# Optimization experiments

Hardware: AMD Instinct MI355X
Metric: run time of the kernel (lower is better)

The kernel has to match this reference:

```python
import jax, jax.numpy as jnp
import numpy as np

N = 100000      # nodes
E = 800000      # edges
F_IN = 128      # input feature dim
HID = 8         # per-head hidden
HEADS = 8
HD = HID * HEADS  # 64
G = 128         # graphs in batch
C = 10          # classes
SLOPE = 0.2     # leaky relu negative slope


def setup_inputs() -> dict:
    key = jax.random.key(0)
    ks = iter(jax.random.split(key, 48))
    def rn(shape, scale=0.1):
        return jax.random.normal(next(ks), shape, jnp.float32) * scale
    inp = {
        'x': jax.random.normal(next(ks), (N, F_IN), jnp.float32),
        'edge_index': jax.random.randint(next(ks), (2, E), 0, N),
        'batch': jnp.sort(jax.random.randint(next(ks), (N,), 0, G)),
        # GAT layer 1
        'W1': rn((F_IN, HEADS * HID)), 'as1': rn((HEADS, HID)), 'ad1': rn((HEADS, HID)), 'b1': jnp.zeros((HEADS * HID,), jnp.float32),
        # GAT layer 2
        'W2': rn((HD, HEADS * HID)), 'as2': rn((HEADS, HID)), 'ad2': rn((HEADS, HID)), 'b2': jnp.zeros((HEADS * HID,), jnp.float32),
        # node attention MLP (HD -> HD//2 -> 2)
        'na_w1': rn((HD, HD // 2)), 'na_b1': jnp.zeros((HD // 2,), jnp.float32), 'na_w2': rn((HD // 2, 2)), 'na_b2': jnp.zeros((2,), jnp.float32),
        # edge attention MLP (2*HD -> HD -> 2)
        'ea_w1': rn((2 * HD, HD)), 'ea_b1': jnp.zeros((HD,), jnp.float32), 'ea_w2': rn((HD, 2)), 'ea_b2': jnp.zeros((2,), jnp.float32),
        # GCN causal / trivial
        'gc_w': rn((HD, HD)), 'gc_b': jnp.zeros((HD,), jnp.float32),
        'gt_w': rn((HD, HD)), 'gt_b': jnp.zeros((HD,), jnp.float32),
        # readouts
        'rc_w': rn((HD, HD)), 'rc_b': jnp.zeros((HD,), jnp.float32),
        'rt_w': rn((HD, HD)), 'rt_b': jnp.zeros((HD,), jnp.float32),
        # classifiers (HD -> HD//2 -> C), combined (2HD -> HD -> C)
        'cc_w1': rn((HD, HD // 2)), 'cc_b1': jnp.zeros((HD // 2,), jnp.float32), 'cc_w2': rn((HD // 2, C)), 'cc_b2': jnp.zeros((C,), jnp.float32),
        'ct_w1': rn((HD, HD // 2)), 'ct_b1': jnp.zeros((HD // 2,), jnp.float32), 'ct_w2': rn((HD // 2, C)), 'ct_b2': jnp.zeros((C,), jnp.float32),
        'cm_w1': rn((2 * HD, HD)), 'cm_b1': jnp.zeros((HD,), jnp.float32), 'cm_w2': rn((HD, C)), 'cm_b2': jnp.zeros((C,), jnp.float32),
    }
    return inp


def _mlp2(h, w1, b1, w2, b2):
    return jax.nn.relu(h @ w1 + b1) @ w2 + b2


def reference(x, edge_index, batch,
              W1, as1, ad1, b1, W2, as2, ad2, b2,
              na_w1, na_b1, na_w2, na_b2,
              ea_w1, ea_b1, ea_w2, ea_b2,
              gc_w, gc_b, gt_w, gt_b,
              rc_w, rc_b, rt_w, rt_b,
              cc_w1, cc_b1, cc_w2, cc_b2,
              ct_w1, ct_b1, ct_w2, ct_b2,
              cm_w1, cm_b1, cm_w2, cm_b2):
    src, dst = edge_index[0], edge_index[1]
    loop = jnp.arange(N)
    s2 = jnp.concatenate([src, loop])  # edges + self-loops (PyG GATConv/GCNConv add self-loops)
    d2 = jnp.concatenate([dst, loop])

    def gat(h_in, W, a_s, a_d, b):
        h = (h_in @ W).reshape(N, HEADS, HID)
        es = jnp.einsum('nhd,hd->nh', h, a_s)
        ed = jnp.einsum('nhd,hd->nh', h, a_d)
        logit = jax.nn.leaky_relu(es[s2] + ed[d2], SLOPE)      # [E+N, H]
        m = jax.ops.segment_max(logit, d2, num_segments=N)
        ex = jnp.exp(logit - m[d2])
        den = jax.ops.segment_sum(ex, d2, num_segments=N)
        alpha = ex / (den[d2] + 1e-16)
        out = jax.ops.segment_sum(h[s2] * alpha[..., None], d2, num_segments=N)
        return out.reshape(N, HEADS * HID) + b

    # GNN encoder (dropout disabled: eval mode)
    H1 = jax.nn.elu(gat(x, W1, as1, ad1, b1))
    H = gat(H1, W2, as2, ad2, b2)                              # [N, HD]

    # node attention
    na = jax.nn.softmax(_mlp2(H, na_w1, na_b1, na_w2, na_b2), axis=1)
    alpha_c, alpha_t = na[:, 0], na[:, 1]
    # edge attention (original edges, no self-loops)
    ef = jnp.concatenate([H[src], H[dst]], axis=1)             # [E, 2*HD]
    ea = jax.nn.softmax(_mlp2(ef, ea_w1, ea_b1, ea_w2, ea_b2), axis=1)
    beta_c, beta_t = ea[:, 0], ea[:, 1]

    Hc = H * alpha_c[:, None]
    Ht = H * alpha_t[:, None]

    def gcn(h_in, w, b, ew):
        # PyG gcn_norm: self-loops with weight 1, symmetric deg^-1/2 normalization
        w_full = jnp.concatenate([ew, jnp.ones((N,), h_in.dtype)])
        deg = jax.ops.segment_sum(w_full, d2, num_segments=N)
        dis = jnp.where(deg > 0, jax.lax.rsqrt(jnp.maximum(deg, 1e-20)), 0.0)
        norm = dis[s2] * w_full * dis[d2]
        h = h_in @ w
        return jax.ops.segment_sum(h[s2] * norm[:, None], d2, num_segments=N) + b

    Gc = gcn(Hc, gc_w, gc_b, beta_c)
    Gt = gcn(Ht, gt_w, gt_b, beta_t)

    # readout: linear then global_add_pool
    hGc = jax.ops.segment_sum(Gc @ rc_w + rc_b, batch, num_segments=G)  # [G, HD]
    hGt = jax.ops.segment_sum(Gt @ rt_w + rt_b, batch, num_segments=G)

    zc = _mlp2(hGc, cc_w1, cc_b1, cc_w2, cc_b2)
    zt = _mlp2(hGt, ct_w1, ct_b1, ct_w2, ct_b2)
    # RandomIntervention: within-graph node shuffle followed by add-pool == plain add-pool
    h_comb = jnp.concatenate([hGc + hGt], axis=1) if False else (hGc + hGt)
    zp = _mlp2(jnp.concatenate([h_comb, jnp.zeros_like(h_comb)], axis=1), cm_w1, cm_b1, cm_w2, cm_b2) if False else _mlp2_comb(h_comb, cm_w1, cm_b1, cm_w2, cm_b2)
    return (zc, zt, zp, hGc, hGt)


def _mlp2_comb(h_comb, cm_w1, cm_b1, cm_w2, cm_b2):
    # original: classifier_combined takes hidden_dim*2 input; forward feeds h_G_c + shuffled_h_G_t
    # which is [G, HD]; to match Linear(2*HD, ...) we use the first HD rows of cm_w1 twice?
    # NO -- the original code as written passes a [G, HD] tensor to a Linear(2*HD, HD) layer,
    # which would error in torch. Faithful runnable interpretation: combined feature is
    # concat([h_G_c, shuffled_h_G_t]) of width 2*HD (the standard CAL formulation).
    return jax.nn.relu(h_comb @ cm_w1 + cm_b1) @ cm_w2 + cm_b2


# clean final definition overriding the commented exploration above
def reference(x, edge_index, batch,
              W1, as1, ad1, b1, W2, as2, ad2, b2,
              na_w1, na_b1, na_w2, na_b2,
              ea_w1, ea_b1, ea_w2, ea_b2,
              gc_w, gc_b, gt_w, gt_b,
              rc_w, rc_b, rt_w, rt_b,
              cc_w1, cc_b1, cc_w2, cc_b2,
              ct_w1, ct_b1, ct_w2, ct_b2,
              cm_w1, cm_b1, cm_w2, cm_b2):
    src, dst = edge_index[0], edge_index[1]
    loop = jnp.arange(N)
    s2 = jnp.concatenate([src, loop])
    d2 = jnp.concatenate([dst, loop])

    def gat(h_in, W, a_s, a_d, b):
        h = (h_in @ W).reshape(N, HEADS, HID)
        es = jnp.einsum('nhd,hd->nh', h, a_s)
        ed = jnp.einsum('nhd,hd->nh', h, a_d)
        logit = jax.nn.leaky_relu(es[s2] + ed[d2], SLOPE)
        m = jax.ops.segment_max(logit, d2, num_segments=N)
        ex = jnp.exp(logit - m[d2])
        den = jax.ops.segment_sum(ex, d2, num_segments=N)
        alpha = ex / (den[d2] + 1e-16)
        out = jax.ops.segment_sum(h[s2] * alpha[..., None], d2, num_segments=N)
        return out.reshape(N, HEADS * HID) + b

    H1 = jax.nn.elu(gat(x, W1, as1, ad1, b1))
    H = gat(H1, W2, as2, ad2, b2)

    na = jax.nn.softmax(_mlp2(H, na_w1, na_b1, na_w2, na_b2), axis=1)
    alpha_c, alpha_t = na[:, 0], na[:, 1]
    ef = jnp.concatenate([H[src], H[dst]], axis=1)
    ea = jax.nn.softmax(_mlp2(ef, ea_w1, ea_b1, ea_w2, ea_b2), axis=1)
    beta_c, beta_t = ea[:, 0], ea[:, 1]

    Hc = H * alpha_c[:, None]
    Ht = H * alpha_t[:, None]

    def gcn(h_in, w, b, ew):
        w_full = jnp.concatenate([ew, jnp.ones((N,), h_in.dtype)])
        deg = jax.ops.segment_sum(w_full, d2, num_segments=N)
        dis = jnp.where(deg > 0, jax.lax.rsqrt(jnp.maximum(deg, 1e-20)), 0.0)
        norm = dis[s2] * w_full * dis[d2]
        h = h_in @ w
        return jax.ops.segment_sum(h[s2] * norm[:, None], d2, num_segments=N) + b

    Gc = gcn(Hc, gc_w, gc_b, beta_c)
    Gt = gcn(Ht, gt_w, gt_b, beta_t)

    hGc = jax.ops.segment_sum(Gc @ rc_w + rc_b, batch, num_segments=G)
    hGt = jax.ops.segment_sum(Gt @ rt_w + rt_b, batch, num_segments=G)

    zc = _mlp2(hGc, cc_w1, cc_b1, cc_w2, cc_b2)
    zt = _mlp2(hGt, ct_w1, ct_b1, ct_w2, ct_b2)
    # RandomIntervention with sorted batch: within-graph permutation + add-pool == add-pool
    h_comb = jnp.concatenate([hGc, hGt], axis=1)  # [G, 2*HD] for Linear(2*HD, ...)
    zp = _mlp2(h_comb, cm_w1, cm_b1, cm_w2, cm_b2)
    return (zc, zt, zp, hGc, hGt)


if __name__ == '__main__':
    out = reference(**setup_inputs())
    print([o.shape for o in out])
```

## Files before the change

kernel.cpp:

```cpp
#include <hip/hip_runtime.h>
#include <hip/hip_bf16.h>

#define N_NODES 100000
#define E_EDGES 800000
#define E2 (E_EDGES + N_NODES)
#define FIN 128
#define HD 64
#define NH 8
#define NG 128
#define NC 10
#define SLOPE 0.2f
#define SELF_FLAG 0x40000000
#define SRC_MASK  0x3FFFFFFF
#define NSCAN_BLK 391
#define NBLK64 1563
#define GB 16
#define ECAP 256
#define NPW 4
#define EA_BLKS 6250

#define U1_STRIPES 261
#define U1_GRID (2 + U1_STRIPES * 7)
#define U1_HISTB (U1_STRIPES * 4)
#define T1 (U1_STRIPES * 3)
#define U2_STRIPES 391
#define U2_GRID (U2_STRIPES * 11)

typedef unsigned short bfu;

__device__ __forceinline__ float lrelu(float x) { return x > 0.f ? x : SLOPE * x; }

__device__ __forceinline__ bfu f2bf(float f) {
    unsigned int u = __float_as_uint(f);
    u += 0x7FFFu + ((u >> 16) & 1u);
    return (bfu)(u >> 16);
}
__device__ __forceinline__ float bf2f(bfu s) {
    return __uint_as_float(((unsigned int)s) << 16);
}
__device__ __forceinline__ float bflo(unsigned int u) { return __uint_as_float(u << 16); }
__device__ __forceinline__ float bfhi(unsigned int u) { return __uint_as_float(u & 0xFFFF0000u); }

template<typename TIN, int KIN, int MODE>
__device__ __forceinline__
void gemm_tile_body(float* smem, int tile,
                    const TIN* __restrict__ in, const float* __restrict__ W,
                    bfu* __restrict__ outB,
                    const float* __restrict__ a_s, const float* __restrict__ a_d,
                    float* __restrict__ es, float* __restrict__ ed)
{
    constexpr int KH = (KIN > 64) ? 64 : KIN;
    constexpr int RS = KIN + 4;
    float* Ws   = smem;
    float* rows = smem + KH * 64;
    int t = threadIdx.x;
    int base = tile * 64;

    if constexpr (sizeof(TIN) == 4) {
        constexpr int RQ = KIN / 4;
        for (int i = t; i < 64 * RQ; i += 256) {
            int r = i / RQ, c = (i % RQ) * 4;
            int n = base + r;
            float4 v = make_float4(0.f, 0.f, 0.f, 0.f);
            if (n < N_NODES) v = *(const float4*)((const float*)in + (size_t)n * KIN + c);
            *(float4*)(rows + r * RS + c) = v;
        }
    } else {
        constexpr int RQ = KIN / 8;
        for (int i = t; i < 64 * RQ; i += 256) {
            int r = i / RQ, c = (i % RQ) * 8;
            int n = base + r;
            uint4 v = make_uint4(0, 0, 0, 0);
            if (n < N_NODES) v = *(const uint4*)((const bfu*)in + (size_t)n * KIN + c);
            float* dp = rows + r * RS + c;
            *(float4*)dp       = make_float4(bflo(v.x), bfhi(v.x), bflo(v.y), bfhi(v.y));
            *(float4*)(dp + 4) = make_float4(bflo(v.z), bfhi(v.z), bflo(v.w), bfhi(v.w));
        }
    }

    int tr = t >> 4, tc = t & 15;
    float acc[4][4] = {};
    const float4* R4 = (const float4*)rows;

    for (int h = 0; h < KIN / KH; ++h) {
        __syncthreads();
        {
            const float4* Wv = (const float4*)(W + (size_t)h * KH * 64);
            float4* Wsv4 = (float4*)Ws;
            for (int i = t; i < KH * 16; i += 256) Wsv4[i] = Wv[i];
        }
        __syncthreads();
        const float4* Wsv = (const float4*)Ws;
#pragma unroll 2
        for (int k = 0; k < KH; k += 4) {
            float4 w0 = Wsv[(k + 0) * 16 + tc];
            float4 w1 = Wsv[(k + 1) * 16 + tc];
            float4 w2 = Wsv[(k + 2) * 16 + tc];
            float4 w3 = Wsv[(k + 3) * 16 + tc];
            int kq = (h * KH + k) >> 2;
#pragma unroll
            for (int i = 0; i < 4; ++i) {
                float4 r = R4[(tr * 4 + i) * (RS / 4) + kq];
                acc[i][0] = fmaf(r.x, w0.x, fmaf(r.y, w1.x, fmaf(r.z, w2.x, fmaf(r.w, w3.x, acc[i][0]))));
                acc[i][1] = fmaf(r.x, w0.y, fmaf(r.y, w1.y, fmaf(r.z, w2.y, fmaf(r.w, w3.y, acc[i][1]))));
                acc[i][2] = fmaf(r.x, w0.z, fmaf(r.y, w1.z, fmaf(r.z, w2.z, fmaf(r.w, w3.z, acc[i][2]))));
                acc[i][3] = fmaf(r.x, w0.w, fmaf(r.y, w1.w, fmaf(r.z, w2.w, fmaf(r.w, w3.w, acc[i][3]))));
            }
        }
    }

    int j0 = tc * 4;
#pragma unroll
    for (int i = 0; i < 4; ++i) {
        int n = base + tr * 4 + i;
        if (n < N_NODES) {
            ushort4 ov;
            ov.x = f2bf(acc[i][0]); ov.y = f2bf(acc[i][1]);
            ov.z = f2bf(acc[i][2]); ov.w = f2bf(acc[i][3]);
            *(ushort4*)(outB + (size_t)n * 64 + j0) = ov;
        }
    }
    if (MODE == 1) {
        float s0[4], s1[4];
#pragma unroll
        for (int i = 0; i < 4; ++i) {
            float pes = 0.f, ped = 0.f;
#pragma unroll
            for (int q = 0; q < 4; ++q) {
                pes = fmaf(acc[i][q], a_s[j0 + q], pes);
                ped = fmaf(acc[i][q], a_d[j0 + q], ped);
            }
            pes += __shfl_xor(pes, 1, 64);
            ped += __shfl_xor(ped, 1, 64);
            s0[i] = pes; s1[i] = ped;
        }
        if ((tc & 1) == 0) {
            int h = tc >> 1;
#pragma unroll
            for (int i = 0; i < 4; ++i) {
                int n = base + tr * 4 + i;
                if (n < N_NODES) {
                    es[n * NH + h] = s0[i];
                    ed[n * NH + h] = s1[i];
                }
            }
        }
    }
}

__device__ __forceinline__
void weight_prep_body(float* smem,
                      const float* __restrict__ gw, const float* __restrict__ gb,
                      const float* __restrict__ rw, const float* __restrict__ rb,
                      float* __restrict__ Wp, float* __restrict__ bp)
{
    float* A = smem;
    float* B = smem + 4096;
    int t = threadIdx.x;
    {
        const float4* ga = (const float4*)gw;
        const float4* rA = (const float4*)rw;
        float4* dA = (float4*)A; float4* dB = (float4*)B;
        for (int i = t; i < 1024; i += 256) { dA[i] = ga[i]; dB[i] = rA[i]; }
    }
    __syncthreads();
    for (int e = t * 16; e < t * 16 + 16; ++e) {
        int k = e >> 6, j = e & 63;
        float acc = 0.f;
#pragma unroll 8
        for (int m = 0; m < 64; ++m) acc = fmaf(A[k * 64 + m], B[m * 64 + j], acc);
        Wp[e] = acc;
    }
    if (t < 64) {
        float acc = rb[t];
#pragma unroll 8
        for (int m = 0; m < 64; ++m) acc = fmaf(gb[m], B[m * 64 + t], acc);
        bp[t] = acc;
    }
}

__global__ __launch_bounds__(256)
void u1_fused(const float* __restrict__ x, const float* __restrict__ W1,
              bfu* __restrict__ B0, const float* __restrict__ as1,
              const float* __restrict__ ad1, float* __restrict__ es,
              float* __restrict__ ed,
              const int* __restrict__ ei, int* __restrict__ cnt,
              int* __restrict__ rank,
              const float* __restrict__ gc_w, const float* __restrict__ gc_b,
              const float* __restrict__ rc_w, const float* __restrict__ rc_b,
              const float* __restrict__ gt_w, const float* __restrict__ gt_b,
              const float* __restrict__ rt_w, const float* __restrict__ rt_b,
              float* __restrict__ Wcp, float* __restrict__ bcp,
              float* __restrict__ Wtp, float* __restrict__ btp)
{
    __shared__ __align__(16) float smem[12544];
    int b = blockIdx.x;
    if (b < 2) {
        if (b == 0) weight_prep_body(smem, gc_w, gc_b, rc_w, rc_b, Wcp, bcp);
        else        weight_prep_body(smem, gt_w, gt_b, rt_w, rt_b, Wtp, btp);
        return;
    }
    int u = b - 2;
    int stripe = u / 7, r = u % 7;
    if (r < 3) {
        gemm_tile_body<float, FIN, 1>(smem, stripe * 3 + r, x, W1, B0, as1, ad1, es, ed);
    } else {
        int idx = stripe * 4 + (r - 3);
        int t = threadIdx.x;
        const int STR = U1_HISTB * 256;
        for (int e = idx * 256 + t; e < E_EDGES; e += 2 * STR) {
            int e1 = e + STR;
            int d0 = ei[E_EDGES + e];
            int r0 = atomicAdd(&cnt[d0], 1);
            int r1 = 0;
            bool has1 = e1 < E_EDGES;
            if (has1) r1 = atomicAdd(&cnt[ei[E_EDGES + e1]], 1);
            rank[e] = r0;
            if (has1) rank[e1] = r1;
        }
    }
}

__global__ __launch_bounds__(256)
void u2_fused(const float* __restrict__ x, const float* __restrict__ W1,
              bfu* __restrict__ B0, const float* __restrict__ as1,
              const float* __restrict__ ad1, float* __restrict__ es,
              float* __restrict__ ed,
              const int* __restrict__ ei, const int* __restrict__ rank,
              const int* __restrict__ offs,
              int* __restrict__ csr)
{
    __shared__ __align__(16) float smem[12544];
    int b = blockIdx.x;
    int stripe = b / 11, r = b % 11;
    int t = threadIdx.x;
    if (r < 8) {
        int e = (stripe * 8 + r) * 256 + t;
        if (e < E_EDGES) {
            int s = ei[e], d = ei[E_EDGES + e];
            csr[offs[d] + rank[e]] = s;
        }
    } else if (r < 10) {
        int tile = T1 + stripe * 2 + (r - 8);
        if (tile < NBLK64)
            gemm_tile_body<float, FIN, 1>(smem, tile, x, W1, B0, as1, ad1, es, ed);
    } else {
        int n = stripe * 256 + t;
        if (n < N_NODES) {
            csr[offs[n + 1] - 1] = n | SELF_FLAG;
        }
    }
}

__global__ __launch_bounds__(256)
void u3_fused(const bfu* __restrict__ in,
              const float* __restrict__ na_w1, const float* __restrict__ na_b1,
              const float* __restrict__ na_w2, const float* __restrict__ na_b2,
              float2* __restrict__ al2,
              const float* __restrict__ ea_w1,
              bfu* __restrict__ out0, bfu* __restrict__ out1)
{
    __shared__ __align__(16) float smem[12544];
    float* Ws   = smem;
    float* rows = smem + 8192;
    int t = threadIdx.x;
    int base = blockIdx.x * 64;
    const float* W0 = ea_w1;
    const float* W1 = ea_w1 + 64 * 64;
    {
        const float4* W0v = (const float4*)W0;
        const float4* W1v = (const float4*)W1;
        float4* Wsv = (float4*)Ws;
        for (int i = t; i < 1024; i += 256) { Wsv[i] = W0v[i]; Wsv[1024 + i] = W1v[i]; }
    }
    for (int i = t; i < 64 * 8; i += 256) {
        int r = i >> 3, c = (i & 7) * 8;
        int n = base + r;
        uint4 v = make_uint4(0, 0, 0, 0);
        if (n < N_NODES) v = *(const uint4*)(in + (size_t)n * 64 + c);
        float* dp = rows + r * 68 + c;
        *(float4*)dp       = make_float4(bflo(v.x), bfhi(v.x), bflo(v.y), bfhi(v.y));
        *(float4*)(dp + 4) = make_float4(bflo(v.z), bfhi(v.z), bflo(v.w), bfhi(v.w));
    }
    __syncthreads();
    {
        int tr = t >> 4, tc = t & 15;
        float a0[4][4] = {}, a1[4][4] = {};
        const float4* Wsv = (const float4*)Ws;
        const float4* R4 = (const float4*)rows;
#pragma unroll 2
        for (int k = 0; k < 64; k += 4) {
            float4 p0 = Wsv[(k + 0) * 16 + tc];
            float4 p1 = Wsv[(k + 1) * 16 + tc];
            float4 p2 = Wsv[(k + 2) * 16 + tc];
            float4 p3 = Wsv[(k + 3) * 16 + tc];
            float4 q0 = Wsv[1024 + (k + 0) * 16 + tc];
            float4 q1 = Wsv[1024 + (k + 1) * 16 + tc];
            float4 q2 = Wsv[1024 + (k + 2) * 16 + tc];
            float4 q3 = Wsv[1024 + (k + 3) * 16 + tc];
            int kq = k >> 2;
#pragma unroll
            for (int i = 0; i < 4; ++i) {
                float4 r = R4[(tr * 4 + i) * 17 + kq];
                a0[i][0] = fmaf(r.x, p0.x, fmaf(r.y, p1.x, fmaf(r.z, p2.x, fmaf(r.w, p3.x, a0[i][0]))));
                a0[i][1] = fmaf(r.x, p0.y, fmaf(r.y, p1.y, fmaf(r.z, p2.y, fmaf(r.w, p3.y, a0[i][1]))));
                a0[i][2] = fmaf(r.x, p0.z, fmaf(r.y, p1.z, fmaf(r.z, p2.z, fmaf(r.w, p3.z, a0[i][2]))));
                a0[i][3] = fmaf(r.x, p0.w, fmaf(r.y, p1.w, fmaf(r.z, p2.w, fmaf(r.w, p3.w, a0[i][3]))));
                a1[i][0] = fmaf(r.x, q0.x, fmaf(r.y, q1.x, fmaf(r.z, q2.x, fmaf(r.w, q3.x, a1[i][0]))));
                a1[i][1] = fmaf(r.x, q0.y, fmaf(r.y, q1.y, fmaf(r.z, q2.y, fmaf(r.w, q3.y, a1[i][1]))));
                a1[i][2] = fmaf(r.x, q0.z, fmaf(r.y, q1.z, fmaf(r.z, q2.z, fmaf(r.w, q3.z, a1[i][2]))));
                a1[i][3] = fmaf(r.x, q0.w, fmaf(r.y, q1.w, fmaf(r.z, q2.w, fmaf(r.w, q3.w, a1[i][3]))));
            }
        }
        int j0 = tc * 4;
#pragma unroll
        for (int i = 0; i < 4; ++i) {
            int n = base + tr * 4 + i;
            if (n >= N_NODES) continue;
            ushort4 o0, o1;
            o0.x = f2bf(a0[i][0]); o0.y = f2bf(a0[i][1]);
            o0.z = f2bf(a0[i][2]); o0.w = f2bf(a0[i][3]);
            o1.x = f2bf(a1[i][0]); o1.y = f2bf(a1[i][1]);
            o1.z = f2bf(a1[i][2]); o1.w = f2bf(a1[i][3]);
            *(ushort4*)(out0 + (size_t)n * 64 + j0) = o0;
            *(ushort4*)(out1 + (size_t)n * 64 + j0) = o1;
        }
    }
    __syncthreads();
    {
        const float4* w1v = (const float4*)na_w1;
        float4* dst = (float4*)Ws;
        for (int i = t; i < 512; i += 256) dst[i] = w1v[i];
        if (t < 64) Ws[2048 + t] = na_w2[t];
    }
    __syncthreads();
    {
        int tr = t >> 3;
        int tc = t & 7;
        float4 bv = *(const float4*)(na_b1 + tc * 4);
        float4 acc0 = bv, acc1 = bv;
        const float4* w1sv = (const float4*)Ws;
#pragma unroll 8
        for (int k = 0; k < 64; ++k) {
            float4 w = w1sv[k * 8 + tc];
            float r0 = rows[tr * 68 + k];
            float r1 = rows[(tr + 32) * 68 + k];
            acc0.x = fmaf(r0, w.x, acc0.x); acc0.y = fmaf(r0, w.y, acc0.y);
            acc0.z = fmaf(r0, w.z, acc0.z); acc0.w = fmaf(r0, w.w, acc0.w);
            acc1.x = fmaf(r1, w.x, acc1.x); acc1.y = fmaf(r1, w.y, acc1.y);
            acc1.z = fmaf(r1, w.z, acc1.z); acc1.w = fmaf(r1, w.w, acc1.w);
        }
        float z00 = 0.f, z01 = 0.f, z10 = 0.f, z11 = 0.f;
        float h0, w20, w21;
        int j0 = tc * 4;
#pragma unroll
        for (int q = 0; q < 4; ++q) {
            float a0q = q == 0 ? acc0.x : q == 1 ? acc0.y : q == 2 ? acc0.z : acc0.w;
            float a1q = q == 0 ? acc1.x : q == 1 ? acc1.y : q == 2 ? acc1.z : acc1.w;
            w20 = Ws[2048 + (j0 + q) * 2]; w21 = Ws[2048 + (j0 + q) * 2 + 1];
            h0 = fmaxf(a0q, 0.f);
            z00 = fmaf(h0, w20, z00); z01 = fmaf(h0, w21, z01);
            h0 = fmaxf(a1q, 0.f);
            z10 = fmaf(h0, w20, z10); z11 = fmaf(h0, w21, z11);
        }
#pragma unroll
        for (int o = 1; o < 8; o <<= 1) {
            z00 += __shfl_xor(z00, o, 64); z01 += __shfl_xor(z01, o, 64);
            z10 += __shfl_xor(z10, o, 64); z11 += __shfl_xor(z11, o, 64);
        }
        if (tc == 0) {
            int n0 = base + tr, n1 = base + tr + 32;
            if (n0 < N_NODES) {
                float zz0 = z00 + na_b2[0], zz1 = z01 + na_b2[1];
                float mx = fmaxf(zz0, zz1);
                float e0 = __expf(zz0 - mx), e1 = __expf(zz1 - mx);
                float ss = e0 + e1;
                al2[n0] = make_float2(e0 / ss, e1 / ss);
            }
            if (n1 < N_NODES) {
                float zz0 = z10 + na_b2[0], zz1 = z11 + na_b2[1];
                float mx = fmaxf(zz0, zz1);
                float e0 = __expf(zz0 - mx), e1 = __expf(zz1 - mx);
                float ss = e0 + e1;
                al2[n1] = make_float2(e0 / ss, e1 / ss);
            }
        }
    }
}

__global__ __launch_bounds__(256)
void gemm_tile_k64(const bfu* __restrict__ in, const float* __restrict__ W,
                   bfu* __restrict__ outB,
                   const float* __restrict__ a_s, const float* __restrict__ a_d,
                   float* __restrict__ es, float* __restrict__ ed)
{
    __shared__ __align__(16) float smem[64 * 64 + 64 * 68];
    gemm_tile_body<bfu, 64, 1>(smem, blockIdx.x, in, W, outB, a_s, a_d, es, ed);
}

__global__ void csr_scan1(const int* __restrict__ cnt, int* __restrict__ offs,
                          int* __restrict__ bsum, const int* __restrict__ batch,
                          int* __restrict__ glo)
{
    __shared__ int tmp[256];
    int t = threadIdx.x;
    int i = blockIdx.x * 256 + t;
    int v = (i < N_NODES) ? cnt[i] + 1 : 0;
    tmp[t] = v; __syncthreads();
#pragma unroll
    for (int o = 1; o < 256; o <<= 1) {
        int a = (t >= o) ? tmp[t - o] : 0;
        __syncthreads();
        tmp[t] += a;
        __syncthreads();
    }
    if (i < N_NODES) offs[i] = tmp[t] - v;
    if (t == 255) bsum[blockIdx.x] = tmp[255];
    if (blockIdx.x == 0 && t <= NG) {
        int l = 0, r = N_NODES;
        while (l < r) { int m = (l + r) >> 1; if (batch[m] < t) l = m + 1; else r = m; }
        glo[t] = l;
    }
}

__global__ void csr_scan23(int* __restrict__ offs, const int* __restrict__ bsum)
{
    __shared__ int tmp[256];
    int b = blockIdx.x;
    int t = threadIdx.x;
    int s = 0;
    for (int j = t; j < b; j += 256) s += bsum[j];
    tmp[t] = s; __syncthreads();
#pragma unroll
    for (int o = 128; o > 0; o >>= 1) {
        if (t < o) tmp[t] += tmp[t + o];
        __syncthreads();
    }
    int prefix = tmp[0];
    int i = b * 256 + t;
    if (i < N_NODES) offs[i] += prefix;
    if (i == 0) offs[N_NODES] = E2;
}

template<int ELU>
__global__ void gat_aggregate4(const int* __restrict__ offs, const int* __restrict__ csr,
                               const float* __restrict__ es, const float* __restrict__ ed,
                               const bfu* __restrict__ hsrcB, const float* __restrict__ bias,
                               bfu* __restrict__ outB)
{
    int n = blockIdx.x * 4 + (threadIdx.x >> 6);
    int lane = threadIdx.x & 63;
    if (n >= N_NODES) return;
    int g  = lane >> 4;
    int fl = lane & 15;
    int h  = fl >> 1;
    int beg = offs[n], end = offs[n + 1];
    float edv = ed[n * NH + h];
    float den = 0.f;
    float4 acc = make_float4(0.f, 0.f, 0.f, 0.f);
    int p = beg + g;
    for (; p + 4 < end; p += 8) {
        int s0 = csr[p] & SRC_MASK;
        int s1 = csr[p + 4] & SRC_MASK;
        float l0 = lrelu(es[s0 * NH + h] + edv);
        float l1 = lrelu(es[s1 * NH + h] + edv);
        float ex0 = __expf(l0);
        float ex1 = __expf(l1);
        den += ex0 + ex1;
        ushort4 ra = *(const ushort4*)(hsrcB + (size_t)s0 * HD + fl * 4);
        ushort4 rb = *(const ushort4*)(hsrcB + (size_t)s1 * HD + fl * 4);
        acc.x = fmaf(bf2f(ra.x), ex0, fmaf(bf2f(rb.x), ex1, acc.x));
        acc.y = fmaf(bf2f(ra.y), ex0, fmaf(bf2f(rb.y), ex1, acc.y));
        acc.z = fmaf(bf2f(ra.z), ex0, fmaf(bf2f(rb.z), ex1, acc.z));
        acc.w = fmaf(bf2f(ra.w), ex0, fmaf(bf2f(rb.w), ex1, acc.w));
    }
    if (p < end) {
        int s = csr[p] & SRC_MASK;
        float l = lrelu(es[s * NH + h] + edv);
        float ex = __expf(l);
        den += ex;
        ushort4 rb = *(const ushort4*)(hsrcB + (size_t)s * HD + fl * 4);
        acc.x = fmaf(bf2f(rb.x), ex, acc.x);
        acc.y = fmaf(bf2f(rb.y), ex, acc.y);
        acc.z = fmaf(bf2f(rb.z), ex, acc.z);
        acc.w = fmaf(bf2f(rb.w), ex, acc.w);
    }
#pragma unroll
    for (int o = 16; o <= 32; o <<= 1) {
        den   += __shfl_xor(den,   o, 64);
        acc.x += __shfl_xor(acc.x, o, 64);
        acc.y += __shfl_xor(acc.y, o, 64);
        acc.z += __shfl_xor(acc.z, o, 64);
        acc.w += __shfl_xor(acc.w, o, 64);
    }
    if (g == 0) {
        float inv = 1.f / (den + 1e-16f);
        float4 bv = *(const float4*)(bias + fl * 4);
        float v0 = acc.x * inv + bv.x;
        float v1 = acc.y * inv + bv.y;
        float v2 = acc.z * inv + bv.z;
        float v3 = acc.w * inv + bv.w;
        if (ELU) {
            v0 = v0 > 0.f ? v0 : (__expf(v0) - 1.f);
            v1 = v1 > 0.f ? v1 : (__expf(v1) - 1.f);
            v2 = v2 > 0.f ? v2 : (__expf(v2) - 1.f);
            v3 = v3 > 0.f ? v3 : (__expf(v3) - 1.f);
        }
        ushort4 ov;
        ov.x = f2bf(v0); ov.y = f2bf(v1); ov.z = f2bf(v2); ov.w = f2bf(v3);
        *(ushort4*)(outB + (size_t)n * HD + fl * 4) = ov;
    }
}

__global__ __launch_bounds__(256)
void edge_att_node(const int* __restrict__ offs, const int* __restrict__ csr,
                   const bfu* __restrict__ P1b, const bfu* __restrict__ P2b,
                   const float* __restrict__ b1, const float* __restrict__ w2,
                   const float* __restrict__ b2,
                   const float2* __restrict__ al2,
                   float2* __restrict__ beta2,
                   float2* __restrict__ prod2)
{
    __shared__ float2 bbuf[4][ECAP];
    int w = threadIdx.x >> 6;
    int lane = threadIdx.x & 63;
    int nbase = (blockIdx.x * 4 + w) * NPW;
    if (nbase >= N_NODES) return;
    int slot = lane >> 3, q = lane & 7;
    const float4* pb = (const float4*)(b1 + q * 8);
    const float4* pw = (const float4*)(w2 + q * 16);
    float4 c0 = pb[0], c1 = pb[1];
    float4 w0 = pw[0], w1v = pw[1], w2v = pw[2], w3v = pw[3];
    float wd0 = w0.x - w0.y,   wd1 = w0.z - w0.w;
    float wd2 = w1v.x - w1v.y, wd3 = w1v.z - w1v.w;
    float wd4 = w2v.x - w2v.y, wd5 = w2v.z - w2v.w;
    float wd6 = w3v.x - w3v.y, wd7 = w3v.z - w3v.w;
    float zbd = b2[0] - b2[1];
    for (int j = 0; j < NPW; ++j) {
        int n = nbase + j;
        if (n >= N_NODES) return;
        uint4 U2 = *(const uint4*)(P2b + (size_t)n * 64 + q * 8);
        float d0 = bflo(U2.x) + c0.x, d1 = bfhi(U2.x) + c0.y;
        float d2 = bflo(U2.y) + c0.z, d3 = bfhi(U2.y) + c0.w;
        float d4 = bflo(U2.z) + c1.x, d5 = bfhi(U2.z) + c1.y;
        float d6 = bflo(U2.w) + c1.z, d7 = bfhi(U2.w) + c1.w;
        int beg = offs[n], endr = offs[n + 1] - 1;
        int m = endr - beg;
        float dc = 0.f, dt = 0.f;
        for (int p = beg + slot; p < endr; p += 8) {
            int s = csr[p];
            uint4 U1 = *(const uint4*)(P1b + (size_t)s * 64 + q * 8);
            float h0 = fmaxf(bflo(U1.x) + d0, 0.f);
            float h1 = fmaxf(bfhi(U1.x) + d1, 0.f);
            float h2 = fmaxf(bflo(U1.y) + d2, 0.f);
            float h3 = fmaxf(bfhi(U1.y) + d3, 0.f);
            float h4 = fmaxf(bflo(U1.z) + d4, 0.f);
            float h5 = fmaxf(bfhi(U1.z) + d5, 0.f);
            float h6 = fmaxf(bflo(U1.w) + d6, 0.f);
            float h7 = fmaxf(bfhi(U1.w) + d7, 0.f);
            float z = fmaf(h0, wd0, fmaf(h1, wd1, fmaf(h2, wd2, fmaf(h3, wd3,
                      fmaf(h4, wd4, fmaf(h5, wd5, fmaf(h6, wd6, h7 * wd7)))))));
            z += __shfl_xor(z, 1, 64);
            z += __shfl_xor(z, 2, 64);
            z += __shfl_xor(z, 4, 64);
            if (q == 0) {
                z += zbd;
                float e = __expf(-fabsf(z));
                float inv = 1.f / (1.f + e);
                float bx = z >= 0.f ? inv : e * inv;
                float by = z >= 0.f ? e * inv : inv;
                int idx = p - beg;
                if (idx < ECAP) bbuf[w][idx] = make_float2(bx, by);
                else            beta2[p]    = make_float2(bx, by);
                dc += bx; dt += by;
            }
        }
        dc += __shfl_xor(dc, 8, 64);  dt += __shfl_xor(dt, 8, 64);
        dc += __shfl_xor(dc, 16, 64); dt += __shfl_xor(dt, 16, 64);
        dc += __shfl_xor(dc, 32, 64); dt += __shfl_xor(dt, 32, 64);
        dc = __shfl(dc, 0, 64); dt = __shfl(dt, 0, 64);
        dc += 1.f; dt += 1.f;
        float ic = rsqrtf(fmaxf(dc, 1e-20f));
        float it = rsqrtf(fmaxf(dt, 1e-20f));
        if (lane == 0) {
            float2 al = al2[n];
            prod2[n] = make_float2(ic * al.x, it * al.y);
        }
        if (m > ECAP)
            asm volatile("s_waitcnt vmcnt(0)" ::: "memory");
        for (int idx = lane; idx <= m; idx += 64) {
            float2 v = (idx == m) ? make_float2(1.f, 1.f)
                     : (idx < ECAP) ? bbuf[w][idx] : beta2[beg + idx];
            beta2[beg + idx] = make_float2(v.x * ic, v.y * it);
        }
    }
}

__global__ __launch_bounds__(256)
void gcn_readout_fused(const int* __restrict__ offs, const int* __restrict__ csr,
                       const int* __restrict__ glo,
                       const bfu* __restrict__ HB,
                       const float2* __restrict__ beta2,
                       const float2* __restrict__ prod2,
                       float* __restrict__ Pc, float* __restrict__ Pt)
{
    int g = blockIdx.x / GB, b = blockIdx.x % GB;
    int t = threadIdx.x;
    int pbeg = offs[glo[g]], pend = offs[glo[g + 1]];
    int total = pend - pbeg;
    int chunk = (total + GB - 1) / GB;
    int start = pbeg + b * chunk;
    int end = start + chunk;
    if (end > pend) end = pend;
    if (start > pend) start = pend;
    int slot = t >> 4, fl = t & 15;
    float4 a1 = make_float4(0.f, 0.f, 0.f, 0.f);
    float4 a2 = make_float4(0.f, 0.f, 0.f, 0.f);
    int p = start + slot;
    for (; p + 48 < end; p += 64) {
#pragma unroll
        for (int j = 0; j < 4; ++j) {
            int pp = p + j * 16;
            int s = csr[pp] & SRC_MASK;
            float2 bb = beta2[pp];
            float2 pr = prod2[s];
            float wc = pr.x * bb.x;
            float wt = pr.y * bb.y;
            ushort4 r0 = *(const ushort4*)(HB + (size_t)s * HD + fl * 4);
            float f0 = bf2f(r0.x), f1 = bf2f(r0.y), f2 = bf2f(r0.z), f3 = bf2f(r0.w);
            a1.x = fmaf(f0, wc, a1.x); a1.y = fmaf(f1, wc, a1.y);
            a1.z = fmaf(f2, wc, a1.z); a1.w = fmaf(f3, wc, a1.w);
            a2.x = fmaf(f0, wt, a2.x); a2.y = fmaf(f1, wt, a2.y);
            a2.z = fmaf(f2, wt, a2.z); a2.w = fmaf(f3, wt, a2.w);
        }
    }
    for (; p < end; p += 16) {
        int s = csr[p] & SRC_MASK;
        float2 bb = beta2[p];
        float2 pr = prod2[s];
        float wc = pr.x * bb.x;
        float wt = pr.y * bb.y;
        ushort4 r0 = *(const ushort4*)(HB + (size_t)s * HD + fl * 4);
        float f0 = bf2f(r0.x), f1 = bf2f(r0.y), f2 = bf2f(r0.z), f3 = bf2f(r0.w);
        a1.x = fmaf(f0, wc, a1.x); a1.y = fmaf(f1, wc, a1.y);
        a1.z = fmaf(f2, wc, a1.z); a1.w = fmaf(f3, wc, a1.w);
        a2.x = fmaf(f0, wt, a2.x); a2.y = fmaf(f1, wt, a2.y);
        a2.z = fmaf(f2, wt, a2.z); a2.w = fmaf(f3, wt, a2.w);
    }
    __shared__ float redc[16 * 64], redt[16 * 64];
    *(float4*)(redc + slot * 64 + fl * 4) = a1;
    *(float4*)(redt + slot * 64 + fl * 4) = a2;
    __syncthreads();
    if (t < 64) {
        float sc = 0.f, st = 0.f;
#pragma unroll
        for (int s = 0; s < 16; ++s) { sc += redc[s * 64 + t]; st += redt[s * 64 + t]; }
        Pc[(size_t)blockIdx.x * 64 + t] = sc;
        Pt[(size_t)blockIdx.x * 64 + t] = st;
    }
}

__global__ __launch_bounds__(64)
void head_final(const float* __restrict__ Pc, const float* __restrict__ Pt,
                const int* __restrict__ glo,
                const float* __restrict__ Wcp, const float* __restrict__ bcp,
                const float* __restrict__ Wtp, const float* __restrict__ btp,
                const float* __restrict__ cc_w1, const float* __restrict__ cc_b1,
                const float* __restrict__ cc_w2, const float* __restrict__ cc_b2,
                const float* __restrict__ ct_w1, const float* __restrict__ ct_b1,
                const float* __restrict__ ct_w2, const float* __restrict__ ct_b2,
                const float* __restrict__ cm_w1, const float* __restrict__ cm_b1,
                const float* __restrict__ cm_w2, const float* __restrict__ cm_b2,
                float* __restrict__ out)
{
    int g = blockIdx.x;
    int t = threadIdx.x;
    __shared__ float scl[64], stl[64], hgc[64], hgt[64], hid[64];
    float sc = 0.f, st = 0.f;
#pragma unroll
    for (int b = 0; b < GB; ++b) {
        sc += Pc[(size_t)(g * GB + b) * 64 + t];
        st += Pt[(size_t)(g * GB + b) * 64 + t];
    }
    scl[t] = sc; stl[t] = st;
    float c = (float)(glo[g + 1] - glo[g]);
    __syncthreads();
    {
        float a = c * bcp[t], bb = c * btp[t];
#pragma unroll 8
        for (int k = 0; k < 64; ++k) {
            a  = fmaf(scl[k], Wcp[k * 64 + t], a);
            bb = fmaf(stl[k], Wtp[k * 64 + t], bb);
        }
        hgc[t] = a; hgt[t] = bb;
        out[3840 + g * 64 + t]  = a;
        out[12032 + g * 64 + t] = bb;
    }
    __syncthreads();
    if (t < 32) {
        float a = cc_b1[t];
#pragma unroll 8
        for (int k = 0; k < 64; ++k) a = fmaf(hgc[k], cc_w1[k * 32 + t], a);
        hid[t] = fmaxf(a, 0.f);
    }
    __syncthreads();
    if (t < NC) {
        float a = cc_b2[t];
#pragma unroll
        for (int k = 0; k < 32; ++k) a = fmaf(hid[k], cc_w2[k * NC + t], a);
        out[g * NC + t] = a;
    }
    __syncthreads();
    if (t < 32) {
        float a = ct_b1[t];
#pragma unroll 8
        for (int k = 0; k < 64; ++k) a = fmaf(hgt[k], ct_w1[k * 32 + t], a);
        hid[t] = fmaxf(a, 0.f);
    }
    __syncthreads();
    if (t < NC) {
        float a = ct_b2[t];
#pragma unroll
        for (int k = 0; k < 32; ++k) a = fmaf(hid[k], ct_w2[k * NC + t], a);
        out[1280 + g * NC + t] = a;
    }
    __syncthreads();
    {
        float a = cm_b1[t];
#pragma unroll 8
        for (int k = 0; k < 64; ++k) {
            a = fmaf(hgc[k], cm_w1[k * 64 + t], a);
            a = fmaf(hgt[k], cm_w1[(64 + k) * 64 + t], a);
        }
        hid[t] = fmaxf(a, 0.f);
    }
    __syncthreads();
    if (t < NC) {
        float a = cm_b2[t];
#pragma unroll 8
        for (int k = 0; k < 64; ++k) a = fmaf(hid[k], cm_w2[k * NC + t], a);
        out[2560 + g * NC + t] = a;
    }
}

extern "C" void kernel_launch(void* const* d_in, const int* in_sizes, int n_in,
                              void* d_out, int out_size, void* d_ws, size_t ws_size,
                              hipStream_t stream)
{
    const float* x     = (const float*)d_in[0];
    const int*   ei    = (const int*)d_in[1];
    const int*   batch = (const int*)d_in[2];
    const float* W1    = (const float*)d_in[3];
    const float* as1   = (const float*)d_in[4];
    const float* ad1   = (const float*)d_in[5];
    const float* b1    = (const float*)d_in[6];
    const float* W2    = (const float*)d_in[7];
    const float* as2   = (const float*)d_in[8];
    const float* ad2   = (const float*)d_in[9];
    const float* b2    = (const float*)d_in[10];
    const float* na_w1 = (const float*)d_in[11];
    const float* na_b1 = (const float*)d_in[12];
    const float* na_w2 = (const float*)d_in[13];
    const float* na_b2 = (const float*)d_in[14];
    const float* ea_w1 = (const float*)d_in[15];
    const float* ea_b1 = (const float*)d_in[16];
    const float* ea_w2 = (const float*)d_in[17];
    const float* ea_b2 = (const float*)d_in[18];
    const float* gc_w  = (const float*)d_in[19];
    const float* gc_b  = (const float*)d_in[20];
    const float* gt_w  = (const float*)d_in[21];
    const float* gt_b  = (const float*)d_in[22];
    const float* rc_w  = (const float*)d_in[23];
    const float* rc_b  = (const float*)d_in[24];
    const float* rt_w  = (const float*)d_in[25];
    const float* rt_b  = (const float*)d_in[26];
    const float* cc_w1 = (const float*)d_in[27];
    const float* cc_b1 = (const float*)d_in[28];
    const float* cc_w2 = (const float*)d_in[29];
    const float* cc_b2 = (const float*)d_in[30];
    const float* ct_w1 = (const float*)d_in[31];
    const float* ct_b1 = (const float*)d_in[32];
    const float* ct_w2 = (const float*)d_in[33];
    const float* ct_b2 = (const float*)d_in[34];
    const float* cm_w1 = (const float*)d_in[35];
    const float* cm_b1 = (const float*)d_in[36];
    const float* cm_w2 = (const float*)d_in[37];
    const float* cm_b2 = (const float*)d_in[38];
    float* out = (float*)d_out;

    float* ws = (float*)d_ws;
    size_t o = 0;
    const size_t nf = (size_t)N_NODES * HD;
    float* es    = ws + o; o += (size_t)N_NODES * NH;
    float* ed    = ws + o; o += (size_t)N_NODES * NH;
    float2* al2  = (float2*)(ws + o); o += (size_t)N_NODES * 2;
    float2* beta2= (float2*)(ws + o); o += (size_t)E2 * 2;
    float2* prod2= (float2*)(ws + o); o += (size_t)N_NODES * 2;
    bfu* B0      = (bfu*)(ws + o); o += nf / 2;
    bfu* B1      = (bfu*)(ws + o); o += nf / 2;
    bfu* B2      = (bfu*)(ws + o); o += nf / 2;
    bfu* BH1     = (bfu*)(ws + o); o += nf / 2;
    int* csr     = (int*)(ws + o); o += E2;
    int* offs    = (int*)(ws + o); o += N_NODES + 1;
    float* Pc    = ws + o; o += (size_t)NG * GB * 64;
    float* Pt    = ws + o; o += (size_t)NG * GB * 64;
    float* Wcp   = ws + o; o += 4096;
    float* Wtp   = ws + o; o += 4096;
    float* bcp   = ws + o; o += 64;
    float* btp   = ws + o; o += 64;
    int* glo     = (int*)(ws + o); o += NG + 2;
    int* cnt  = (int*)beta2;
    int* bsum = (int*)prod2;
    int* rank = (int*)B1;

    const int NW_BLKS = N_NODES / 4;

    hipMemsetAsync(cnt, 0, (size_t)N_NODES * 4, stream);
    u1_fused<<<U1_GRID, 256, 0, stream>>>(x, W1, B0, as1, ad1, es, ed,
                                          ei, cnt, rank,
                                          gc_w, gc_b, rc_w, rc_b,
                                          gt_w, gt_b, rt_w, rt_b,
                                          Wcp, bcp, Wtp, btp);
    csr_scan1<<<NSCAN_BLK, 256, 0, stream>>>(cnt, offs, bsum, batch, glo);
    csr_scan23<<<NSCAN_BLK, 256, 0, stream>>>(offs, bsum);

    u2_fused<<<U2_GRID, 256, 0, stream>>>(x, W1, B0, as1, ad1, es, ed,
                                          ei, rank, offs, csr);

    gat_aggregate4<1><<<NW_BLKS, 256, 0, stream>>>(offs, csr, es, ed, B0, b1, BH1);

    gemm_tile_k64<<<NBLK64, 256, 0, stream>>>(BH1, W2, B0, as2, ad2, es, ed);
    gat_aggregate4<0><<<NW_BLKS, 256, 0, stream>>>(offs, csr, es, ed, B0, b2, B2);

    u3_fused<<<NBLK64, 256, 0, stream>>>(B2, na_w1, na_b1, na_w2, na_b2, al2,
                                         ea_w1, B0, B1);

    edge_att_node<<<EA_BLKS, 256, 0, stream>>>(offs, csr, B0, B1,
                                               ea_b1, ea_w2, ea_b2, al2,
                                               beta2, prod2);

    gcn_readout_fused<<<NG * GB, 256, 0, stream>>>(offs, csr, glo, B2,
                                                   beta2, prod2, Pc, Pt);

    head_final<<<NG, 64, 0, stream>>>(Pc, Pt, glo,
                                      Wcp, bcp, Wtp, btp,
                                      cc_w1, cc_b1, cc_w2, cc_b2,
                                      ct_w1, ct_b1, ct_w2, ct_b2,
                                      cm_w1, cm_b1, cm_w2, cm_b2, out);
    (void)in_sizes; (void)n_in; (void)out_size; (void)ws_size;
}
```

Baseline: 465.5 us.

## Assign one 16-lane group per node in GAT aggregation instead of a whole wave

The GAT aggregation kernel used to give each node a full 64-lane wave, splitting that node's edges across four 16-lane groups and combining them with cross-lane shuffles. Now each 16-lane group owns its own node and walks all of its edges, two per iteration, so a block covers 16 nodes and the grid shrinks by four. This drops the shuffle reduction and the idle lanes during the write-out, and gives more independent nodes per wave. In exchange each group walks a longer serial edge chain, and groups in the same wave diverge when node degrees differ.

```diff
diff --git a/kernel.cpp b/kernel.cpp
--- a/kernel.cpp
+++ b/kernel.cpp
@@ -18,6 +18,7 @@
 #define ECAP 256
 #define NPW 4
 #define EA_BLKS 6250
+#define AG_BLKS 6250
 
 #define U1_STRIPES 261
 #define U1_GRID (2 + U1_STRIPES * 7)
@@ -448,24 +449,24 @@
                                const bfu* __restrict__ hsrcB, const float* __restrict__ bias,
                                bfu* __restrict__ outB)
 {
-    int n = blockIdx.x * 4 + (threadIdx.x >> 6);
+    int w = threadIdx.x >> 6;
     int lane = threadIdx.x & 63;
-    if (n >= N_NODES) return;
-    int g  = lane >> 4;
+    int slot = lane >> 4;
     int fl = lane & 15;
     int h  = fl >> 1;
+    int n = (blockIdx.x * 4 + w) * 4 + slot;
+    if (n >= N_NODES) return;
+    float4 bv = *(const float4*)(bias + fl * 4);
     int beg = offs[n], end = offs[n + 1];
     float edv = ed[n * NH + h];
     float den = 0.f;
     float4 acc = make_float4(0.f, 0.f, 0.f, 0.f);
-    int p = beg + g;
-    for (; p + 4 < end; p += 8) {
+    int p = beg;
+    for (; p + 1 < end; p += 2) {
         int s0 = csr[p] & SRC_MASK;
-        int s1 = csr[p + 4] & SRC_MASK;
-        float l0 = lrelu(es[s0 * NH + h] + edv);
-        float l1 = lrelu(es[s1 * NH + h] + edv);
-        float ex0 = __expf(l0);
-        float ex1 = __expf(l1);
+        int s1 = csr[p + 1] & SRC_MASK;
+        float ex0 = __expf(lrelu(es[s0 * NH + h] + edv));
+        float ex1 = __expf(lrelu(es[s1 * NH + h] + edv));
         den += ex0 + ex1;
         ushort4 ra = *(const ushort4*)(hsrcB + (size_t)s0 * HD + fl * 4);
         ushort4 rb = *(const ushort4*)(hsrcB + (size_t)s1 * HD + fl * 4);
@@ -476,8 +477,7 @@
     }
     if (p < end) {
         int s = csr[p] & SRC_MASK;
-        float l = lrelu(es[s * NH + h] + edv);
-        float ex = __expf(l);
+        float ex = __expf(lrelu(es[s * NH + h] + edv));
         den += ex;
         ushort4 rb = *(const ushort4*)(hsrcB + (size_t)s * HD + fl * 4);
         acc.x = fmaf(bf2f(rb.x), ex, acc.x);
@@ -485,31 +485,20 @@
         acc.z = fmaf(bf2f(rb.z), ex, acc.z);
         acc.w = fmaf(bf2f(rb.w), ex, acc.w);
     }
-#pragma unroll
-    for (int o = 16; o <= 32; o <<= 1) {
-        den   += __shfl_xor(den,   o, 64);
-        acc.x += __shfl_xor(acc.x, o, 64);
-        acc.y += __shfl_xor(acc.y, o, 64);
-        acc.z += __shfl_xor(acc.z, o, 64);
-        acc.w += __shfl_xor(acc.w, o, 64);
-    }
-    if (g == 0) {
-        float inv = 1.f / (den + 1e-16f);
-        float4 bv = *(const float4*)(bias + fl * 4);
-        float v0 = acc.x * inv + bv.x;
-        float v1 = acc.y * inv + bv.y;
-        float v2 = acc.z * inv + bv.z;
-        float v3 = acc.w * inv + bv.w;
-        if (ELU) {
-            v0 = v0 > 0.f ? v0 : (__expf(v0) - 1.f);
-            v1 = v1 > 0.f ? v1 : (__expf(v1) - 1.f);
-            v2 = v2 > 0.f ? v2 : (__expf(v2) - 1.f);
-            v3 = v3 > 0.f ? v3 : (__expf(v3) - 1.f);
-        }
-        ushort4 ov;
-        ov.x = f2bf(v0); ov.y = f2bf(v1); ov.z = f2bf(v2); ov.w = f2bf(v3);
-        *(ushort4*)(outB + (size_t)n * HD + fl * 4) = ov;
-    }
+    float inv = 1.f / (den + 1e-16f);
+    float v0 = acc.x * inv + bv.x;
+    float v1 = acc.y * inv + bv.y;
+    float v2 = acc.z * inv + bv.z;
+    float v3 = acc.w * inv + bv.w;
+    if (ELU) {
+        v0 = v0 > 0.f ? v0 : (__expf(v0) - 1.f);
+        v1 = v1 > 0.f ? v1 : (__expf(v1) - 1.f);
+        v2 = v2 > 0.f ? v2 : (__expf(v2) - 1.f);
+        v3 = v3 > 0.f ? v3 : (__expf(v3) - 1.f);
+    }
+    ushort4 ov;
+    ov.x = f2bf(v0); ov.y = f2bf(v1); ov.z = f2bf(v2); ov.w = f2bf(v3);
+    *(ushort4*)(outB + (size_t)n * HD + fl * 4) = ov;
 }
 
 __global__ __launch_bounds__(256)
@@ -813,8 +802,6 @@
     int* bsum = (int*)prod2;
     int* rank = (int*)B1;
 
-    const int NW_BLKS = N_NODES / 4;
-
     hipMemsetAsync(cnt, 0, (size_t)N_NODES * 4, stream);
     u1_fused<<<U1_GRID, 256, 0, stream>>>(x, W1, B0, as1, ad1, es, ed,
                                           ei, cnt, rank,
@@ -827,10 +814,10 @@
     u2_fused<<<U2_GRID, 256, 0, stream>>>(x, W1, B0, as1, ad1, es, ed,
                                           ei, rank, offs, csr);
 
-    gat_aggregate4<1><<<NW_BLKS, 256, 0, stream>>>(offs, csr, es, ed, B0, b1, BH1);
+    gat_aggregate4<1><<<AG_BLKS, 256, 0, stream>>>(offs, csr, es, ed, B0, b1, BH1);
 
     gemm_tile_k64<<<NBLK64, 256, 0, stream>>>(BH1, W2, B0, as2, ad2, es, ed);
-    gat_aggregate4<0><<<NW_BLKS, 256, 0, stream>>>(offs, csr, es, ed, B0, b2, B2);
+    gat_aggregate4<0><<<AG_BLKS, 256, 0, stream>>>(offs, csr, es, ed, B0, b2, B2);
 
     u3_fused<<<NBLK64, 256, 0, stream>>>(B2, na_w1, na_b1, na_w2, na_b2, al2,
                                          ea_w1, B0, B1);
```

After: 446.0 us. 1.04x faster.
